# Kernel tuning notes

Hardware: AMD Instinct MI355X
Metric: run time of the kernel (lower is better)

The kernel has to match this reference:

```python
import jax, jax.numpy as jnp
import numpy as np
import math

SEQ = 2048
N_EMBD = 2048
N_HEAD = 16
DIM = N_EMBD // N_HEAD  # 128


def setup_inputs() -> dict:
    key = jax.random.key(0)
    k1, k2, k3, k4, k5 = jax.random.split(key, 5)
    s = 1.0 / math.sqrt(N_EMBD)
    return {
        "hidden_states": jax.random.normal(k1, (SEQ, N_EMBD), dtype=jnp.float32),
        "Wqkv": jax.random.normal(k2, (N_HEAD, N_EMBD, 3 * DIM), dtype=jnp.float32) * s,
        "bqkv": jax.random.normal(k3, (N_HEAD, 3 * DIM), dtype=jnp.float32) * 0.02,
        "Wout": jax.random.normal(k4, (N_EMBD, N_EMBD), dtype=jnp.float32) * s,
        "bout": jax.random.normal(k5, (N_EMBD,), dtype=jnp.float32) * 0.02,
    }


def reference(hidden_states, Wqkv, bqkv, Wout, bout):
    # per-head qkv projection: [h, s, 3*dim]
    qkv = jnp.einsum("se,hed->hsd", hidden_states, Wqkv) + bqkv[:, None, :]
    q, k, v = qkv[..., :DIM], qkv[..., DIM:2 * DIM], qkv[..., 2 * DIM:]
    # NOTE: original divides by sqrt(n_embd), not sqrt(head_dim)
    scale = 1.0 / math.sqrt(N_EMBD)
    scores = jnp.einsum("hsd,htd->hst", q, k) * scale  # [h, s, s]
    causal = jnp.tril(jnp.ones((SEQ, SEQ), dtype=bool))
    scores = jnp.where(causal[None], scores, -jnp.inf)
    probs = jax.nn.softmax(scores, axis=-1)
    out = jnp.einsum("hst,htd->hsd", probs, v)  # [h, s, dim]
    out = jnp.transpose(out, (1, 0, 2)).reshape(SEQ, N_EMBD)  # concat heads
    return out @ Wout + bout
```

## Files before the change

### kernel.cpp

```cpp
#include <hip/hip_runtime.h>
#include <cfloat>

#define SEQ   2048
#define NE    2048
#define NH    16
#define DIM   128
#define NKV   384
#define QSCALE 0.022097086912079611f

typedef __attribute__((ext_vector_type(8))) short bf16x8;
typedef __attribute__((ext_vector_type(4))) float f32x4;
typedef __attribute__((ext_vector_type(16))) float f32x16;
typedef __attribute__((ext_vector_type(8))) unsigned short u16x8;
typedef __attribute__((ext_vector_type(4))) unsigned int u32x4;
typedef __attribute__((ext_vector_type(2))) unsigned int u32x2;

#define PSLOT_B 16896u
#define NUNITS  768

__device__ __forceinline__ unsigned short f32_to_bf16_rn(float x) {
    unsigned u = __builtin_bit_cast(unsigned, x);
    u += 0x7fffu + ((u >> 16) & 1u);
    return (unsigned short)(u >> 16);
}

__device__ __forceinline__ unsigned cvt_pk_bf16(float lo, float hi) {
    unsigned r;
    asm("v_cvt_pk_bf16_f32 %0, %1, %2" : "=v"(r) : "v"(lo), "v"(hi));
    return r;
}
__device__ __forceinline__ float bf16lo(unsigned w) {
    return __builtin_bit_cast(float, w << 16);
}
__device__ __forceinline__ float bf16hi(unsigned w) {
    return __builtin_bit_cast(float, w & 0xFFFF0000u);
}

__device__ __forceinline__ void gload16(const void* g, void* l) {
    __builtin_amdgcn_global_load_lds(
        (const __attribute__((address_space(1))) unsigned int*)g,
        (__attribute__((address_space(3))) unsigned int*)l, 16, 0, 0);
}

__global__ __launch_bounds__(256) void convert_bf16_kernel(
    const float* __restrict__ src, unsigned short* __restrict__ dst, int n4)
{
    for (int i = blockIdx.x * 256 + threadIdx.x; i < n4; i += gridDim.x * 256) {
        float4 x = ((const float4*)src)[i];
        ushort4 h;
        h.x = f32_to_bf16_rn(x.x);
        h.y = f32_to_bf16_rn(x.y);
        h.z = f32_to_bf16_rn(x.z);
        h.w = f32_to_bf16_rn(x.w);
        ((ushort4*)dst)[i] = h;
    }
}

__global__ __launch_bounds__(256) void transpose_bf16_kernel(
    const float* __restrict__ src, unsigned short* __restrict__ dst, int K, int N)
{
    const int kt = blockIdx.x, nt = blockIdx.y, b = blockIdx.z;
    const float* s = src + (size_t)b * K * N;
    __shared__ float tile[64][65];
    const int tid = threadIdx.x;
    #pragma unroll
    for (int i = 0; i < 4; i++) {
        int idx = tid + 256 * i;
        int kk = idx >> 4, n4 = idx & 15;
        float4 val = *(const float4*)&s[(size_t)(kt * 64 + kk) * N + nt * 64 + n4 * 4];
        tile[kk][n4 * 4 + 0] = val.x; tile[kk][n4 * 4 + 1] = val.y;
        tile[kk][n4 * 4 + 2] = val.z; tile[kk][n4 * 4 + 3] = val.w;
    }
    __syncthreads();
    #pragma unroll
    for (int i = 0; i < 2; i++) {
        int idx = tid + 256 * i;
        int nn = idx >> 3, k8 = idx & 7;
        u16x8 hv;
        #pragma unroll
        for (int j = 0; j < 8; j++)
            hv[j] = f32_to_bf16_rn(tile[k8 * 8 + j][nn]);
        size_t off = ((size_t)b * N + nt * 64 + nn) * K + kt * 64 + k8 * 8;
        *(u16x8*)&dst[off] = hv;
    }
}

__global__ __launch_bounds__(256, 4) void gemm_qkv_kernel(
    const unsigned short* __restrict__ A, const unsigned short* __restrict__ B,
    const float* __restrict__ bias,
    unsigned short* __restrict__ o0, unsigned short* __restrict__ o1,
    unsigned short* __restrict__ o2)
{
    __shared__ unsigned short smem[2][128][64];
    const int tid = threadIdx.x;
    const int wave = tid >> 6, lane = tid & 63;
    const int s0 = blockIdx.x * 128, n0 = blockIdx.y * 128, z = blockIdx.z;
    const int bRowBase = z * NKV + n0;

    const int srow = lane >> 3;
    const int sswz = ((lane & 7) ^ srow) << 4;
    size_t aoff[4], boff[4];
    #pragma unroll
    for (int j = 0; j < 4; j++) {
        int ra = s0 + wave * 32 + j * 8 + srow;
        int rb = bRowBase + wave * 32 + j * 8 + srow;
        aoff[j] = 2 * ((size_t)ra * NE) + sswz;
        boff[j] = 2 * ((size_t)rb * NE) + sswz;
    }
    const char* pA = (const char*)A;
    const char* pB = (const char*)B;

    f32x4 acc[4][4];
    #pragma unroll
    for (int i = 0; i < 4; i++)
        #pragma unroll
        for (int j = 0; j < 4; j++) acc[i][j] = (f32x4){0.f, 0.f, 0.f, 0.f};

    const int wm = wave >> 1, wn = wave & 1;
    const int fr = lane & 15, kg = lane >> 4;

    for (int k0 = 0; k0 < NE; k0 += 64) {
        #pragma unroll
        for (int j = 0; j < 4; j++) {
            gload16(pA + aoff[j], &smem[0][wave * 32 + j * 8][0]);
            gload16(pB + boff[j], &smem[1][wave * 32 + j * 8][0]);
            aoff[j] += 128; boff[j] += 128;
        }
        __syncthreads();

        #pragma unroll
        for (int kh = 0; kh < 2; kh++) {
            bf16x8 af[4], bf[4];
            #pragma unroll
            for (int f = 0; f < 4; f++) {
                int ra = wm * 64 + f * 16 + fr;
                int ca = ((kh * 4 + kg) ^ (ra & 7)) << 4;
                af[f] = *(const bf16x8*)((const char*)&smem[0][0][0] + ra * 128 + ca);
                int rb = wn * 64 + f * 16 + fr;
                int cb = ((kh * 4 + kg) ^ (rb & 7)) << 4;
                bf[f] = *(const bf16x8*)((const char*)&smem[1][0][0] + rb * 128 + cb);
            }
            #pragma unroll
            for (int fm = 0; fm < 4; fm++)
                #pragma unroll
                for (int fn = 0; fn < 4; fn++)
                    acc[fm][fn] = __builtin_amdgcn_mfma_f32_16x16x32_bf16(
                        af[fm], bf[fn], acc[fm][fn], 0, 0, 0);
        }
        __syncthreads();
    }

    #pragma unroll
    for (int fm = 0; fm < 4; fm++)
        #pragma unroll
        for (int fn = 0; fn < 4; fn++) {
            int col = wn * 64 + fn * 16 + fr;
            int row = wm * 64 + fm * 16 + kg * 4;
            const int seg = n0 >> 7;
            unsigned short* dst = (seg == 0) ? o0 : ((seg == 1) ? o1 : o2);
            const float mult = (seg == 0) ? QSCALE : 1.f;
            float bv = bias[z * NKV + n0 + col];
            #pragma unroll
            for (int r = 0; r < 4; r++)
                dst[((size_t)(z * SEQ + s0 + row + r)) * DIM + col] =
                    f32_to_bf16_rn((acc[fm][fn][r] + bv) * mult);
        }
}

__global__ __launch_bounds__(128, 3) void gemm_out_kernel(
    const unsigned short* __restrict__ A, const unsigned short* __restrict__ B,
    const float* __restrict__ bias, float* __restrict__ out)
{
    __shared__ unsigned short As[64][64];
    __shared__ unsigned short Bs[128][64];
    const int tid = threadIdx.x;
    const int wave = tid >> 6, lane = tid & 63;
    const int s0 = blockIdx.x * 64, n0 = blockIdx.y * 128;

    const int srow = lane >> 3;
    const int sswz = ((lane & 7) ^ srow) << 4;
    size_t aof[4], boff[4], boff2[4];
    #pragma unroll
    for (int j = 0; j < 4; j++) {
        int ra = s0 + wave * 32 + j * 8 + srow;
        aof[j] = 2 * ((size_t)ra * NE) + sswz;
        int rb = n0 + wave * 64 + j * 8 + srow;
        boff[j] = 2 * ((size_t)rb * NE) + sswz;
        int rb2 = n0 + wave * 64 + 32 + j * 8 + srow;
        boff2[j] = 2 * ((size_t)rb2 * NE) + sswz;
    }
    const char* pA = (const char*)A;
    const char* pB = (const char*)B;

    f32x4 acc[4][4];
    #pragma unroll
    for (int i = 0; i < 4; i++)
        #pragma unroll
        for (int j = 0; j < 4; j++) acc[i][j] = (f32x4){0.f, 0.f, 0.f, 0.f};

    const int fr = lane & 15, kg = lane >> 4;

    for (int k0 = 0; k0 < NE; k0 += 64) {
        #pragma unroll
        for (int j = 0; j < 4; j++) {
            gload16(pA + aof[j], &As[wave * 32 + j * 8][0]);
            gload16(pB + boff[j], &Bs[wave * 64 + j * 8][0]);
            gload16(pB + boff2[j], &Bs[wave * 64 + 32 + j * 8][0]);
            aof[j] += 128; boff[j] += 128; boff2[j] += 128;
        }
        __syncthreads();

        #pragma unroll
        for (int kh = 0; kh < 2; kh++) {
            bf16x8 af[4], bf[4];
            #pragma unroll
            for (int f = 0; f < 4; f++) {
                int ra = f * 16 + fr;
                int ca = ((kh * 4 + kg) ^ (ra & 7)) << 4;
                af[f] = *(const bf16x8*)((const char*)&As[0][0] + ra * 128 + ca);
                int rb = wave * 64 + f * 16 + fr;
                int cb = ((kh * 4 + kg) ^ (rb & 7)) << 4;
                bf[f] = *(const bf16x8*)((const char*)&Bs[0][0] + rb * 128 + cb);
            }
            #pragma unroll
            for (int fm = 0; fm < 4; fm++)
                #pragma unroll
                for (int fn = 0; fn < 4; fn++)
                    acc[fm][fn] = __builtin_amdgcn_mfma_f32_16x16x32_bf16(
                        af[fm], bf[fn], acc[fm][fn], 0, 0, 0);
        }
        __syncthreads();
    }

    #pragma unroll
    for (int fm = 0; fm < 4; fm++)
        #pragma unroll
        for (int fn = 0; fn < 4; fn++) {
            int col = n0 + wave * 64 + fn * 16 + fr;
            int row = s0 + fm * 16 + kg * 4;
            float bv = bias[col];
            #pragma unroll
            for (int r = 0; r < 4; r++)
                out[(size_t)(row + r) * NE + col] = acc[fm][fn][r] + bv;
        }
}

__global__ __launch_bounds__(128, 2) void attn_partial_kernel(
    const unsigned short* __restrict__ Qb, const unsigned short* __restrict__ Kb,
    const unsigned short* __restrict__ Vb, char* __restrict__ partB,
    unsigned short* __restrict__ AOb)
{
    const int uid = (int)blockIdx.x;
    const int h = uid & 15;
    const int u = uid >> 4;
    int qt, t_begin, t_end, chunk;
    bool direct;
    if (u < 16) {
        qt = 16 + u; t_begin = 0; t_end = 16; chunk = 0; direct = false;
    } else {
        int p = (u - 16) >> 1;
        if (((u - 16) & 1) == 0) { qt = 15 - p; t_begin = 0; t_end = qt + 1; chunk = 0; direct = true; }
        else                     { qt = 31 - p; t_begin = 16; t_end = qt + 1; chunk = 1; direct = false; }
    }
    char* slotB = partB + (size_t)((h * 16 + (qt - 16)) * 2 + chunk) * PSLOT_B;

    const char* kh = (const char*)(Kb + (size_t)h * SEQ * DIM);
    const unsigned short* vh = Vb + (size_t)h * SEQ * DIM;

    __shared__ __align__(16) unsigned short Klds[64 * 128];
    __shared__ __align__(16) unsigned short Vt[128][72];

    const int tid = threadIdx.x;
    const int w = tid >> 6, lane = tid & 63;
    const int cc = lane & 31, hh = lane >> 5;
    const int Q0 = qt * 64 + w * 32;

    bf16x8 qf[8];
    {
        const unsigned short* qrow = Qb + ((size_t)h * SEQ + Q0 + cc) * DIM;
        #pragma unroll
        for (int st = 0; st < 8; st++)
            qf[st] = *(const bf16x8*)&qrow[st * 16 + hh * 8];
    }

    const int key0 = (tid & 31) * 2;
    const int dbase = (tid >> 5) * 32;

    f32x16 oacc[4];
    #pragma unroll
    for (int dt = 0; dt < 4; dt++)
        #pragma unroll
        for (int r = 0; r < 16; r++) oacc[dt][r] = 0.f;
    float m_run = -FLT_MAX, l_run = 0.f;

    u16x8 vrA[4], vrB[4];

    {
        const int tb0 = t_begin * 64;
        #pragma unroll
        for (int j = 0; j < 8; j++) {
            int row = w * 32 + j * 4 + (lane >> 4);
            gload16(kh + (size_t)(tb0 + row) * 256 + (((lane & 15) ^ (row & 7)) << 4),
                    &Klds[(w * 32 + j * 4) * 128]);
        }
        const u16x8* p0 = (const u16x8*)&vh[(size_t)(tb0 + key0) * DIM + dbase];
        const u16x8* p1 = (const u16x8*)&vh[(size_t)(tb0 + key0 + 1) * DIM + dbase];
        #pragma unroll
        for (int q8 = 0; q8 < 4; q8++) { vrA[q8] = p0[q8]; vrB[q8] = p1[q8]; }
        #pragma unroll
        for (int q8 = 0; q8 < 4; q8++)
            #pragma unroll
            for (int j = 0; j < 8; j++)
                *(unsigned*)&Vt[dbase + q8 * 8 + j][key0] =
                    (unsigned)(unsigned short)vrA[q8][j] |
                    ((unsigned)(unsigned short)vrB[q8][j] << 16);
        asm volatile("s_waitcnt vmcnt(0)" ::: "memory");
        __syncthreads();
    }

    for (int t = t_begin; t < t_end; t++) {
        const int t0 = t * 64;
        const bool notlast = (t + 1 < t_end);
        const int t1 = t0 + 64;

        if (notlast) {
            const u16x8* p0 = (const u16x8*)&vh[(size_t)(t1 + key0) * DIM + dbase];
            const u16x8* p1 = (const u16x8*)&vh[(size_t)(t1 + key0 + 1) * DIM + dbase];
            #pragma unroll
            for (int q8 = 0; q8 < 4; q8++) { vrA[q8] = p0[q8]; vrB[q8] = p1[q8]; }
        }

        f32x16 s0, s1;
        #pragma unroll
        for (int r = 0; r < 16; r++) { s0[r] = 0.f; s1[r] = 0.f; }
        __builtin_amdgcn_s_setprio(1);
        #pragma unroll
        for (int st = 0; st < 8; st++) {
            int r0 = cc, r1 = 32 + cc;
            bf16x8 kf0 = *(const bf16x8*)((const char*)&Klds[0] +
                            r0 * 256 + (((2 * st + hh) ^ (r0 & 7)) << 4));
            bf16x8 kf1 = *(const bf16x8*)((const char*)&Klds[0] +
                            r1 * 256 + (((2 * st + hh) ^ (r1 & 7)) << 4));
            s0 = __builtin_amdgcn_mfma_f32_32x32x16_bf16(kf0, qf[st], s0, 0, 0, 0);
            s1 = __builtin_amdgcn_mfma_f32_32x32x16_bf16(kf1, qf[st], s1, 0, 0, 0);
        }
        __builtin_amdgcn_s_setprio(0);

        if (t == qt) {
            const int q = Q0 + cc;
            #pragma unroll
            for (int r = 0; r < 16; r++) {
                int krow = (r & 3) + 8 * (r >> 2) + 4 * hh;
                s0[r] = (t0 + krow > q) ? -3.0e38f : s0[r];
                s1[r] = (t0 + 32 + krow > q) ? -3.0e38f : s1[r];
            }
        }

        float t4[4];
        #pragma unroll
        for (int j = 0; j < 4; j++) t4[j] = fmaxf(s0[j], s1[j]);
        #pragma unroll
        for (int r = 4; r < 16; r++) t4[r & 3] = fmaxf(t4[r & 3], fmaxf(s0[r], s1[r]));
        float mx = fmaxf(fmaxf(t4[0], t4[1]), fmaxf(t4[2], t4[3]));
        mx = fmaxf(mx, __shfl_xor(mx, 32));
        const bool nog = __all((int)(mx - m_run <= 8.f));
        float sc = 1.f;
        if (!nog) {
            float m_new = fmaxf(m_run, mx);
            sc = __expf(m_run - m_new);
            m_run = m_new;
        }

        float e4[4] = {0.f, 0.f, 0.f, 0.f};
        #pragma unroll
        for (int r = 0; r < 16; r++) {
            s0[r] = __expf(s0[r] - m_run);
            s1[r] = __expf(s1[r] - m_run);
            e4[r & 3] += s0[r] + s1[r];
        }
        float psum = (e4[0] + e4[1]) + (e4[2] + e4[3]);
        psum += __shfl_xor(psum, 32);
        l_run = l_run * sc + psum;
        if (!nog) {
            #pragma unroll
            for (int dt = 0; dt < 4; dt++)
                #pragma unroll
                for (int r = 0; r < 16; r++) oacc[dt][r] *= sc;
        }

        unsigned pd[16];
        #pragma unroll
        for (int uu = 0; uu < 8; uu++) {
            pd[uu]     = cvt_pk_bf16(s0[2 * uu], s0[2 * uu + 1]);
            pd[8 + uu] = cvt_pk_bf16(s1[2 * uu], s1[2 * uu + 1]);
        }

        __builtin_amdgcn_s_setprio(1);
        #pragma unroll
        for (int km = 0; km < 4; km++) {
            u32x2 sA = __builtin_amdgcn_permlane32_swap(pd[4 * km + 0], pd[4 * km + 2], false, false);
            u32x2 sB = __builtin_amdgcn_permlane32_swap(pd[4 * km + 1], pd[4 * km + 3], false, false);
            u32x4 pw; pw[0] = sA[0]; pw[1] = sB[0]; pw[2] = sA[1]; pw[3] = sB[1];
            bf16x8 pb = __builtin_bit_cast(bf16x8, pw);
            #pragma unroll
            for (int dt = 0; dt < 4; dt++) {
                bf16x8 vf = *(const bf16x8*)&Vt[dt * 32 + cc][km * 16 + hh * 8];
                oacc[dt] = __builtin_amdgcn_mfma_f32_32x32x16_bf16(vf, pb, oacc[dt], 0, 0, 0);
            }
        }
        __builtin_amdgcn_s_setprio(0);

        if (notlast) {
            __syncthreads();
            #pragma unroll
            for (int j = 0; j < 8; j++) {
                int row = w * 32 + j * 4 + (lane >> 4);
                gload16(kh + (size_t)(t1 + row) * 256 + (((lane & 15) ^ (row & 7)) << 4),
                        &Klds[(w * 32 + j * 4) * 128]);
            }
            #pragma unroll
            for (int q8 = 0; q8 < 4; q8++)
                #pragma unroll
                for (int j = 0; j < 8; j++)
                    *(unsigned*)&Vt[dbase + q8 * 8 + j][key0] =
                        (unsigned)(unsigned short)vrA[q8][j] |
                        ((unsigned)(unsigned short)vrB[q8][j] << 16);
            asm volatile("s_waitcnt vmcnt(0)" ::: "memory");
            __syncthreads();
        }
    }

    const int prow = w * 32 + cc;
    const float inv = 1.f / l_run;
    if (direct) {
        unsigned short* aorow = AOb + (size_t)(Q0 + cc) * NE + h * DIM;
        #pragma unroll
        for (int dt = 0; dt < 4; dt++)
            #pragma unroll
            for (int m = 0; m < 4; m++) {
                unsigned lo = cvt_pk_bf16(oacc[dt][4 * m + 0] * inv, oacc[dt][4 * m + 1] * inv);
                unsigned hi = cvt_pk_bf16(oacc[dt][4 * m + 2] * inv, oacc[dt][4 * m + 3] * inv);
                u32x2 pk; pk[0] = lo; pk[1] = hi;
                *(u32x2*)&aorow[dt * 32 + 8 * m + 4 * hh] = pk;
            }
    } else {
        float* mf = (float*)slotB;
        float* lf = mf + 64;
        if (hh == 0) { mf[prow] = m_run; lf[prow] = l_run; }
        unsigned short* orow = (unsigned short*)(slotB + 512) + (size_t)prow * 128;
        #pragma unroll
        for (int dt = 0; dt < 4; dt++)
            #pragma unroll
            for (int m = 0; m < 4; m++) {
                unsigned lo = cvt_pk_bf16(oacc[dt][4 * m + 0] * inv, oacc[dt][4 * m + 1] * inv);
                unsigned hi = cvt_pk_bf16(oacc[dt][4 * m + 2] * inv, oacc[dt][4 * m + 3] * inv);
                u32x2 pk; pk[0] = lo; pk[1] = hi;
                *(u32x2*)&orow[dt * 32 + 8 * m + 4 * hh] = pk;
            }
    }
}

__global__ __launch_bounds__(128) void attn_merge_kernel(
    const char* __restrict__ partB, unsigned short* __restrict__ AOb)
{
    const int blk = (int)blockIdx.x;
    const int h = blk >> 4, qtm = blk & 15;
    const char* s0B = partB + (size_t)((h * 16 + qtm) * 2) * PSLOT_B;
    const char* s1B = s0B + PSLOT_B;
    const float* m0 = (const float*)s0B; const float* l0 = m0 + 64;
    const float* m1 = (const float*)s1B; const float* l1 = m1 + 64;
    const unsigned short* O0 = (const unsigned short*)(s0B + 512);
    const unsigned short* O1 = (const unsigned short*)(s1B + 512);

    const int tid = threadIdx.x;
    const int f4 = tid & 31;
    const int rg = tid >> 5;

    #pragma unroll 1
    for (int j = 0; j < 16; j++) {
        const int row = rg + 4 * j;
        float M = fmaxf(m0[row], m1[row]);
        float w0 = __expf(m0[row] - M) * l0[row];
        float w1 = __expf(m1[row] - M) * l1[row];
        float inv = 1.f / (w0 + w1);
        w0 *= inv; w1 *= inv;
        u32x2 a = *(const u32x2*)&O0[(size_t)row * 128 + f4 * 4];
        u32x2 b = *(const u32x2*)&O1[(size_t)row * 128 + f4 * 4];
        float r0 = w0 * bf16lo(a[0]) + w1 * bf16lo(b[0]);
        float r1 = w0 * bf16hi(a[0]) + w1 * bf16hi(b[0]);
        float r2 = w0 * bf16lo(a[1]) + w1 * bf16lo(b[1]);
        float r3 = w0 * bf16hi(a[1]) + w1 * bf16hi(b[1]);
        u32x2 pk; pk[0] = cvt_pk_bf16(r0, r1); pk[1] = cvt_pk_bf16(r2, r3);
        *(u32x2*)&AOb[(size_t)((16 + qtm) * 64 + row) * NE + h * DIM + f4 * 4] = pk;
    }
}

extern "C" void kernel_launch(void* const* d_in, const int* in_sizes, int n_in,
                              void* d_out, int out_size, void* d_ws, size_t ws_size,
                              hipStream_t stream) {
    const float* H    = (const float*)d_in[0];
    const float* Wqkv = (const float*)d_in[1];
    const float* bqkv = (const float*)d_in[2];
    const float* Wout = (const float*)d_in[3];
    const float* bout = (const float*)d_in[4];
    float* out = (float*)d_out;

    char* W8 = (char*)d_ws;
    const size_t MiB = 1ull << 20;
    unsigned short* qb  = (unsigned short*)(W8 + 0);
    unsigned short* kb  = (unsigned short*)(W8 + 8 * MiB);
    unsigned short* vb  = (unsigned short*)(W8 + 16 * MiB);
    unsigned short* Wob = (unsigned short*)(W8 + 24 * MiB);
    unsigned short* AOb = (unsigned short*)(W8 + 32 * MiB);
    char* part          = (char*)(W8 + 40 * MiB);
    unsigned short* Hb  = (unsigned short*)(W8 + 49 * MiB);
    unsigned short* Wqb = (unsigned short*)(W8 + 57 * MiB);

    convert_bf16_kernel<<<1024, 256, 0, stream>>>(H, Hb, SEQ * NE / 4);
    transpose_bf16_kernel<<<dim3(NE / 64, NKV / 64, NH), 256, 0, stream>>>(
        Wqkv, Wqb, NE, NKV);
    transpose_bf16_kernel<<<dim3(NE / 64, NE / 64, 1), 256, 0, stream>>>(
        Wout, Wob, NE, NE);
    gemm_qkv_kernel<<<dim3(SEQ / 128, NKV / 128, NH), 256, 0, stream>>>(
        Hb, Wqb, bqkv, qb, kb, vb);
    attn_partial_kernel<<<dim3(NUNITS), 128, 0, stream>>>(qb, kb, vb, part, AOb);
    attn_merge_kernel<<<dim3(256), 128, 0, stream>>>(part, AOb);
    gemm_out_kernel<<<dim3(SEQ / 64, NE / 128), 128, 0, stream>>>(
        AOb, Wob, bout, out);
}
```

Baseline: 167.8 us.

## Enlarge attention query tile to 128 rows with 4 waves sharing K/V tiles

The attention partial kernel now processes 128 query rows per block with 256 threads instead of 64 rows with 128 threads. Each K/V tile loaded into LDS is reused by four waves rather than two, which halves global K/V traffic and the number of blocks. The causal mask condition, partial-slot layout and merge kernel are adjusted for the larger tile. In exchange there are fewer blocks (384), coarser load balancing across the causal triangle, and more masked work on diagonal tiles.

Result: slower. 190.9 us (+13.8%).

```diff
diff --git a/kernel.cpp b/kernel.cpp
--- a/kernel.cpp
+++ b/kernel.cpp
@@ -15,8 +15,8 @@
 typedef __attribute__((ext_vector_type(4))) unsigned int u32x4;
 typedef __attribute__((ext_vector_type(2))) unsigned int u32x2;
 
-#define PSLOT_B 16896u
-#define NUNITS  768
+#define PSLOT_B 33792u
+#define NUNITS  384
 
 __device__ __forceinline__ unsigned short f32_to_bf16_rn(float x) {
     unsigned u = __builtin_bit_cast(unsigned, x);
@@ -245,7 +245,7 @@
         }
 }
 
-__global__ __launch_bounds__(128, 2) void attn_partial_kernel(
+__global__ __launch_bounds__(256, 3) void attn_partial_kernel(
     const unsigned short* __restrict__ Qb, const unsigned short* __restrict__ Kb,
     const unsigned short* __restrict__ Vb, char* __restrict__ partB,
     unsigned short* __restrict__ AOb)
@@ -253,16 +253,17 @@
     const int uid = (int)blockIdx.x;
     const int h = uid & 15;
     const int u = uid >> 4;
-    int qt, t_begin, t_end, chunk;
+    int qb, t_begin, t_end, chunk;
     bool direct;
-    if (u < 16) {
-        qt = 16 + u; t_begin = 0; t_end = 16; chunk = 0; direct = false;
+    if (u < 8) {
+        qb = 8 + u; t_begin = 0; t_end = 16; chunk = 0; direct = false;
     } else {
-        int p = (u - 16) >> 1;
-        if (((u - 16) & 1) == 0) { qt = 15 - p; t_begin = 0; t_end = qt + 1; chunk = 0; direct = true; }
-        else                     { qt = 31 - p; t_begin = 16; t_end = qt + 1; chunk = 1; direct = false; }
-    }
-    char* slotB = partB + (size_t)((h * 16 + (qt - 16)) * 2 + chunk) * PSLOT_B;
+        int p = (u - 8) >> 1;
+        if (((u - 8) & 1) == 0) { qb = 7 - p;  t_begin = 0;  t_end = 2 * qb + 2; chunk = 0; direct = true; }
+        else                    { qb = 15 - p; t_begin = 16; t_end = 2 * qb + 2; chunk = 1; direct = false; }
+    }
+    const int sidx = direct ? 0 : ((h * 8 + (qb - 8)) * 2 + chunk);
+    char* slotB = partB + (size_t)sidx * PSLOT_B;
 
     const char* kh = (const char*)(Kb + (size_t)h * SEQ * DIM);
     const unsigned short* vh = Vb + (size_t)h * SEQ * DIM;
@@ -273,7 +274,7 @@
     const int tid = threadIdx.x;
     const int w = tid >> 6, lane = tid & 63;
     const int cc = lane & 31, hh = lane >> 5;
-    const int Q0 = qt * 64 + w * 32;
+    const int Q0 = qb * 128 + w * 32;
 
     bf16x8 qf[8];
     {
@@ -284,7 +285,7 @@
     }
 
     const int key0 = (tid & 31) * 2;
-    const int dbase = (tid >> 5) * 32;
+    const int dbase = (tid >> 5) * 16;
 
     f32x16 oacc[4];
     #pragma unroll
@@ -293,27 +294,26 @@
         for (int r = 0; r < 16; r++) oacc[dt][r] = 0.f;
     float m_run = -FLT_MAX, l_run = 0.f;
 
-    u16x8 vrA[4], vrB[4];
+    u16x8 vrA[2], vrB[2];
 
     {
         const int tb0 = t_begin * 64;
         #pragma unroll
-        for (int j = 0; j < 8; j++) {
-            int row = w * 32 + j * 4 + (lane >> 4);
+        for (int j = 0; j < 4; j++) {
+            int row = w * 16 + j * 4 + (lane >> 4);
             gload16(kh + (size_t)(tb0 + row) * 256 + (((lane & 15) ^ (row & 7)) << 4),
-                    &Klds[(w * 32 + j * 4) * 128]);
+                    &Klds[(w * 16 + j * 4) * 128]);
         }
         const u16x8* p0 = (const u16x8*)&vh[(size_t)(tb0 + key0) * DIM + dbase];
         const u16x8* p1 = (const u16x8*)&vh[(size_t)(tb0 + key0 + 1) * DIM + dbase];
-        #pragma unroll
-        for (int q8 = 0; q8 < 4; q8++) { vrA[q8] = p0[q8]; vrB[q8] = p1[q8]; }
-        #pragma unroll
-        for (int q8 = 0; q8 < 4; q8++)
+        vrA[0] = p0[0]; vrA[1] = p0[1]; vrB[0] = p1[0]; vrB[1] = p1[1];
+        #pragma unroll
+        for (int g = 0; g < 2; g++)
             #pragma unroll
             for (int j = 0; j < 8; j++)
-                *(unsigned*)&Vt[dbase + q8 * 8 + j][key0] =
-                    (unsigned)(unsigned short)vrA[q8][j] |
-                    ((unsigned)(unsigned short)vrB[q8][j] << 16);
+                *(unsigned*)&Vt[dbase + g * 8 + j][key0] =
+                    (unsigned)(unsigned short)vrA[g][j] |
+                    ((unsigned)(unsigned short)vrB[g][j] << 16);
         asm volatile("s_waitcnt vmcnt(0)" ::: "memory");
         __syncthreads();
     }
@@ -326,8 +326,7 @@
         if (notlast) {
             const u16x8* p0 = (const u16x8*)&vh[(size_t)(t1 + key0) * DIM + dbase];
             const u16x8* p1 = (const u16x8*)&vh[(size_t)(t1 + key0 + 1) * DIM + dbase];
-            #pragma unroll
-            for (int q8 = 0; q8 < 4; q8++) { vrA[q8] = p0[q8]; vrB[q8] = p1[q8]; }
+            vrA[0] = p0[0]; vrA[1] = p0[1]; vrB[0] = p1[0]; vrB[1] = p1[1];
         }
 
         f32x16 s0, s1;
@@ -346,7 +345,7 @@
         }
         __builtin_amdgcn_s_setprio(0);
 
-        if (t == qt) {
+        if (t0 + 63 > Q0) {
             const int q = Q0 + cc;
             #pragma unroll
             for (int r = 0; r < 16; r++) {
@@ -413,18 +412,18 @@
         if (notlast) {
             __syncthreads();
             #pragma unroll
-            for (int j = 0; j < 8; j++) {
-                int row = w * 32 + j * 4 + (lane >> 4);
+            for (int j = 0; j < 4; j++) {
+                int row = w * 16 + j * 4 + (lane >> 4);
                 gload16(kh + (size_t)(t1 + row) * 256 + (((lane & 15) ^ (row & 7)) << 4),
-                        &Klds[(w * 32 + j * 4) * 128]);
-            }
-            #pragma unroll
-            for (int q8 = 0; q8 < 4; q8++)
+                        &Klds[(w * 16 + j * 4) * 128]);
+            }
+            #pragma unroll
+            for (int g = 0; g < 2; g++)
                 #pragma unroll
                 for (int j = 0; j < 8; j++)
-                    *(unsigned*)&Vt[dbase + q8 * 8 + j][key0] =
-                        (unsigned)(unsigned short)vrA[q8][j] |
-                        ((unsigned)(unsigned short)vrB[q8][j] << 16);
+                    *(unsigned*)&Vt[dbase + g * 8 + j][key0] =
+                        (unsigned)(unsigned short)vrA[g][j] |
+                        ((unsigned)(unsigned short)vrB[g][j] << 16);
             asm volatile("s_waitcnt vmcnt(0)" ::: "memory");
             __syncthreads();
         }
@@ -445,9 +444,9 @@
             }
     } else {
         float* mf = (float*)slotB;
-        float* lf = mf + 64;
+        float* lf = mf + 128;
         if (hh == 0) { mf[prow] = m_run; lf[prow] = l_run; }
-        unsigned short* orow = (unsigned short*)(slotB + 512) + (size_t)prow * 128;
+        unsigned short* orow = (unsigned short*)(slotB + 1024) + (size_t)prow * 128;
         #pragma unroll
         for (int dt = 0; dt < 4; dt++)
             #pragma unroll
@@ -464,20 +463,20 @@
     const char* __restrict__ partB, unsigned short* __restrict__ AOb)
 {
     const int blk = (int)blockIdx.x;
-    const int h = blk >> 4, qtm = blk & 15;
-    const char* s0B = partB + (size_t)((h * 16 + qtm) * 2) * PSLOT_B;
+    const int h = blk >> 3, qbm = blk & 7;
+    const char* s0B = partB + (size_t)((h * 8 + qbm) * 2) * PSLOT_B;
     const char* s1B = s0B + PSLOT_B;
-    const float* m0 = (const float*)s0B; const float* l0 = m0 + 64;
-    const float* m1 = (const float*)s1B; const float* l1 = m1 + 64;
-    const unsigned short* O0 = (const unsigned short*)(s0B + 512);
-    const unsigned short* O1 = (const unsigned short*)(s1B + 512);
+    const float* m0 = (const float*)s0B; const float* l0 = m0 + 128;
+    const float* m1 = (const float*)s1B; const float* l1 = m1 + 128;
+    const unsigned short* O0 = (const unsigned short*)(s0B + 1024);
+    const unsigned short* O1 = (const unsigned short*)(s1B + 1024);
 
     const int tid = threadIdx.x;
     const int f4 = tid & 31;
     const int rg = tid >> 5;
 
     #pragma unroll 1
-    for (int j = 0; j < 16; j++) {
+    for (int j = 0; j < 32; j++) {
         const int row = rg + 4 * j;
         float M = fmaxf(m0[row], m1[row]);
         float w0 = __expf(m0[row] - M) * l0[row];
@@ -491,7 +490,7 @@
         float r2 = w0 * bf16lo(a[1]) + w1 * bf16lo(b[1]);
         float r3 = w0 * bf16hi(a[1]) + w1 * bf16hi(b[1]);
         u32x2 pk; pk[0] = cvt_pk_bf16(r0, r1); pk[1] = cvt_pk_bf16(r2, r3);
-        *(u32x2*)&AOb[(size_t)((16 + qtm) * 64 + row) * NE + h * DIM + f4 * 4] = pk;
+        *(u32x2*)&AOb[(size_t)((8 + qbm) * 128 + row) * NE + h * DIM + f4 * 4] = pk;
     }
 }
 
@@ -523,8 +522,8 @@
         Wout, Wob, NE, NE);
     gemm_qkv_kernel<<<dim3(SEQ / 128, NKV / 128, NH), 256, 0, stream>>>(
         Hb, Wqb, bqkv, qb, kb, vb);
-    attn_partial_kernel<<<dim3(NUNITS), 128, 0, stream>>>(qb, kb, vb, part, AOb);
-    attn_merge_kernel<<<dim3(256), 128, 0, stream>>>(part, AOb);
+    attn_partial_kernel<<<dim3(NUNITS), 256, 0, stream>>>(qb, kb, vb, part, AOb);
+    attn_merge_kernel<<<dim3(128), 128, 0, stream>>>(part, AOb);
     gemm_out_kernel<<<dim3(SEQ / 64, NE / 128), 128, 0, stream>>>(
         AOb, Wob, bout, out);
 }
```

## Emit V pre-transposed from QKV GEMM and async-load it; fuse prep kernels

Applied to the files above, without the earlier changes.

The QKV GEMM epilogue now writes V in a head-major transposed [dim][seq] layout. The attention kernel can then stream V tiles straight into swizzled LDS with global_load_lds, instead of loading into registers and transposing through scalar LDS stores each iteration. The three input conversion and transpose kernels are also merged into one launch to cut launch overhead. The trade-offs are V epilogue stores that are strided along SEQ, and a larger bf16-to-fp32 conversion blob in a single kernel.

Measured after the change: 159.3 us. 5.1% less time.

```diff
diff --git a/kernel.cpp b/kernel.cpp
--- a/kernel.cpp
+++ b/kernel.cpp
@@ -42,32 +42,15 @@
         (__attribute__((address_space(3))) unsigned int*)l, 16, 0, 0);
 }
 
-__global__ __launch_bounds__(256) void convert_bf16_kernel(
-    const float* __restrict__ src, unsigned short* __restrict__ dst, int n4)
+__device__ __forceinline__ void transpose_tile_64(
+    const float* __restrict__ src, unsigned short* __restrict__ dst,
+    int K, int N, int kt, int nt, float (*tile)[65], int tid)
 {
-    for (int i = blockIdx.x * 256 + threadIdx.x; i < n4; i += gridDim.x * 256) {
-        float4 x = ((const float4*)src)[i];
-        ushort4 h;
-        h.x = f32_to_bf16_rn(x.x);
-        h.y = f32_to_bf16_rn(x.y);
-        h.z = f32_to_bf16_rn(x.z);
-        h.w = f32_to_bf16_rn(x.w);
-        ((ushort4*)dst)[i] = h;
-    }
-}
-
-__global__ __launch_bounds__(256) void transpose_bf16_kernel(
-    const float* __restrict__ src, unsigned short* __restrict__ dst, int K, int N)
-{
-    const int kt = blockIdx.x, nt = blockIdx.y, b = blockIdx.z;
-    const float* s = src + (size_t)b * K * N;
-    __shared__ float tile[64][65];
-    const int tid = threadIdx.x;
     #pragma unroll
     for (int i = 0; i < 4; i++) {
         int idx = tid + 256 * i;
         int kk = idx >> 4, n4 = idx & 15;
-        float4 val = *(const float4*)&s[(size_t)(kt * 64 + kk) * N + nt * 64 + n4 * 4];
+        float4 val = *(const float4*)&src[(size_t)(kt * 64 + kk) * N + nt * 64 + n4 * 4];
         tile[kk][n4 * 4 + 0] = val.x; tile[kk][n4 * 4 + 1] = val.y;
         tile[kk][n4 * 4 + 2] = val.z; tile[kk][n4 * 4 + 3] = val.w;
     }
@@ -80,8 +63,44 @@
         #pragma unroll
         for (int j = 0; j < 8; j++)
             hv[j] = f32_to_bf16_rn(tile[k8 * 8 + j][nn]);
-        size_t off = ((size_t)b * N + nt * 64 + nn) * K + kt * 64 + k8 * 8;
+        size_t off = (size_t)(nt * 64 + nn) * K + kt * 64 + k8 * 8;
         *(u16x8*)&dst[off] = hv;
+    }
+}
+
+__global__ __launch_bounds__(256) void prep_kernel(
+    const float* __restrict__ H, const float* __restrict__ Wqkv,
+    const float* __restrict__ Wout,
+    unsigned short* __restrict__ Hb, unsigned short* __restrict__ Wqb,
+    unsigned short* __restrict__ Wob)
+{
+    __shared__ float tile[64][65];
+    const int b = (int)blockIdx.x;
+    const int tid = threadIdx.x;
+    if (b < 1024) {
+        const int n4 = SEQ * NE / 4;
+        for (int i = b * 256 + tid; i < n4; i += 1024 * 256) {
+            float4 x = ((const float4*)H)[i];
+            ushort4 h;
+            h.x = f32_to_bf16_rn(x.x);
+            h.y = f32_to_bf16_rn(x.y);
+            h.z = f32_to_bf16_rn(x.z);
+            h.w = f32_to_bf16_rn(x.w);
+            ((ushort4*)Hb)[i] = h;
+        }
+    } else if (b < 4096) {
+        const int idx = b - 1024;
+        const int kt = idx & 31;
+        const int nt = (idx >> 5) % 6;
+        const int hh = (idx >> 5) / 6;
+        transpose_tile_64(Wqkv + (size_t)hh * NE * NKV,
+                          Wqb + (size_t)hh * NKV * NE,
+                          NE, NKV, kt, nt, tile, tid);
+    } else {
+        const int idx = b - 4096;
+        const int kt = idx & 31;
+        const int nt = idx >> 5;
+        transpose_tile_64(Wout, Wob, NE, NE, kt, nt, tile, tid);
     }
 }
 
@@ -150,20 +169,27 @@
         __syncthreads();
     }
 
+    const int seg = n0 >> 7;
     #pragma unroll
     for (int fm = 0; fm < 4; fm++)
         #pragma unroll
         for (int fn = 0; fn < 4; fn++) {
             int col = wn * 64 + fn * 16 + fr;
             int row = wm * 64 + fm * 16 + kg * 4;
-            const int seg = n0 >> 7;
-            unsigned short* dst = (seg == 0) ? o0 : ((seg == 1) ? o1 : o2);
-            const float mult = (seg == 0) ? QSCALE : 1.f;
             float bv = bias[z * NKV + n0 + col];
-            #pragma unroll
-            for (int r = 0; r < 4; r++)
-                dst[((size_t)(z * SEQ + s0 + row + r)) * DIM + col] =
-                    f32_to_bf16_rn((acc[fm][fn][r] + bv) * mult);
+            if (seg == 2) {
+                unsigned lo = cvt_pk_bf16(acc[fm][fn][0] + bv, acc[fm][fn][1] + bv);
+                unsigned hi = cvt_pk_bf16(acc[fm][fn][2] + bv, acc[fm][fn][3] + bv);
+                u32x2 pk; pk[0] = lo; pk[1] = hi;
+                *(u32x2*)&o2[((size_t)z * DIM + col) * SEQ + s0 + row] = pk;
+            } else {
+                unsigned short* dst = (seg == 0) ? o0 : o1;
+                const float mult = (seg == 0) ? QSCALE : 1.f;
+                #pragma unroll
+                for (int r = 0; r < 4; r++)
+                    dst[((size_t)(z * SEQ + s0 + row + r)) * DIM + col] =
+                        f32_to_bf16_rn((acc[fm][fn][r] + bv) * mult);
+            }
         }
 }
 
@@ -247,7 +273,7 @@
 
 __global__ __launch_bounds__(128, 2) void attn_partial_kernel(
     const unsigned short* __restrict__ Qb, const unsigned short* __restrict__ Kb,
-    const unsigned short* __restrict__ Vb, char* __restrict__ partB,
+    const unsigned short* __restrict__ VTb, char* __restrict__ partB,
     unsigned short* __restrict__ AOb)
 {
     const int uid = (int)blockIdx.x;
@@ -264,11 +290,11 @@
     }
     char* slotB = partB + (size_t)((h * 16 + (qt - 16)) * 2 + chunk) * PSLOT_B;
 
-    const char* kh = (const char*)(Kb + (size_t)h * SEQ * DIM);
-    const unsigned short* vh = Vb + (size_t)h * SEQ * DIM;
+    const char* kh  = (const char*)(Kb + (size_t)h * SEQ * DIM);
+    const char* vth = (const char*)(VTb + (size_t)h * DIM * SEQ);
 
     __shared__ __align__(16) unsigned short Klds[64 * 128];
-    __shared__ __align__(16) unsigned short Vt[128][72];
+    __shared__ __align__(16) unsigned short Vt[128 * 64];
 
     const int tid = threadIdx.x;
     const int w = tid >> 6, lane = tid & 63;
@@ -283,8 +309,10 @@
             qf[st] = *(const bf16x8*)&qrow[st * 16 + hh * 8];
     }
 
-    const int key0 = (tid & 31) * 2;
-    const int dbase = (tid >> 5) * 32;
+    const int k_row4 = lane >> 4;
+    const int k_slot = lane & 15;
+    const int v_row8 = lane >> 3;
+    const int v_slot = lane & 7;
 
     f32x16 oacc[4];
     #pragma unroll
@@ -293,27 +321,20 @@
         for (int r = 0; r < 16; r++) oacc[dt][r] = 0.f;
     float m_run = -FLT_MAX, l_run = 0.f;
 
-    u16x8 vrA[4], vrB[4];
-
     {
         const int tb0 = t_begin * 64;
         #pragma unroll
         for (int j = 0; j < 8; j++) {
-            int row = w * 32 + j * 4 + (lane >> 4);
-            gload16(kh + (size_t)(tb0 + row) * 256 + (((lane & 15) ^ (row & 7)) << 4),
+            int row = w * 32 + j * 4 + k_row4;
+            gload16(kh + (size_t)(tb0 + row) * 256 + ((k_slot ^ (row & 7)) << 4),
                     &Klds[(w * 32 + j * 4) * 128]);
         }
-        const u16x8* p0 = (const u16x8*)&vh[(size_t)(tb0 + key0) * DIM + dbase];
-        const u16x8* p1 = (const u16x8*)&vh[(size_t)(tb0 + key0 + 1) * DIM + dbase];
-        #pragma unroll
-        for (int q8 = 0; q8 < 4; q8++) { vrA[q8] = p0[q8]; vrB[q8] = p1[q8]; }
-        #pragma unroll
-        for (int q8 = 0; q8 < 4; q8++)
-            #pragma unroll
-            for (int j = 0; j < 8; j++)
-                *(unsigned*)&Vt[dbase + q8 * 8 + j][key0] =
-                    (unsigned)(unsigned short)vrA[q8][j] |
-                    ((unsigned)(unsigned short)vrB[q8][j] << 16);
+        #pragma unroll
+        for (int j = 0; j < 8; j++) {
+            int row = w * 64 + j * 8 + v_row8;
+            gload16(vth + (size_t)row * (SEQ * 2) + tb0 * 2 + ((v_slot ^ (row & 7)) << 4),
+                    &Vt[(w * 64 + j * 8) * 64]);
+        }
         asm volatile("s_waitcnt vmcnt(0)" ::: "memory");
         __syncthreads();
     }
@@ -322,13 +343,6 @@
         const int t0 = t * 64;
         const bool notlast = (t + 1 < t_end);
         const int t1 = t0 + 64;
-
-        if (notlast) {
-            const u16x8* p0 = (const u16x8*)&vh[(size_t)(t1 + key0) * DIM + dbase];
-            const u16x8* p1 = (const u16x8*)&vh[(size_t)(t1 + key0 + 1) * DIM + dbase];
-            #pragma unroll
-            for (int q8 = 0; q8 < 4; q8++) { vrA[q8] = p0[q8]; vrB[q8] = p1[q8]; }
-        }
 
         f32x16 s0, s1;
         #pragma unroll
@@ -404,7 +418,9 @@
             bf16x8 pb = __builtin_bit_cast(bf16x8, pw);
             #pragma unroll
             for (int dt = 0; dt < 4; dt++) {
-                bf16x8 vf = *(const bf16x8*)&Vt[dt * 32 + cc][km * 16 + hh * 8];
+                int d = dt * 32 + cc;
+                bf16x8 vf = *(const bf16x8*)((const char*)&Vt[0] +
+                                d * 128 + (((km * 2 + hh) ^ (d & 7)) << 4));
                 oacc[dt] = __builtin_amdgcn_mfma_f32_32x32x16_bf16(vf, pb, oacc[dt], 0, 0, 0);
             }
         }
@@ -414,17 +430,16 @@
             __syncthreads();
             #pragma unroll
             for (int j = 0; j < 8; j++) {
-                int row = w * 32 + j * 4 + (lane >> 4);
-                gload16(kh + (size_t)(t1 + row) * 256 + (((lane & 15) ^ (row & 7)) << 4),
+                int row = w * 32 + j * 4 + k_row4;
+                gload16(kh + (size_t)(t1 + row) * 256 + ((k_slot ^ (row & 7)) << 4),
                         &Klds[(w * 32 + j * 4) * 128]);
             }
             #pragma unroll
-            for (int q8 = 0; q8 < 4; q8++)
-                #pragma unroll
-                for (int j = 0; j < 8; j++)
-                    *(unsigned*)&Vt[dbase + q8 * 8 + j][key0] =
-                        (unsigned)(unsigned short)vrA[q8][j] |
-                        ((unsigned)(unsigned short)vrB[q8][j] << 16);
+            for (int j = 0; j < 8; j++) {
+                int row = w * 64 + j * 8 + v_row8;
+                gload16(vth + (size_t)row * (SEQ * 2) + t1 * 2 + ((v_slot ^ (row & 7)) << 4),
+                        &Vt[(w * 64 + j * 8) * 64]);
+            }
             asm volatile("s_waitcnt vmcnt(0)" ::: "memory");
             __syncthreads();
         }
@@ -509,21 +524,17 @@
     const size_t MiB = 1ull << 20;
     unsigned short* qb  = (unsigned short*)(W8 + 0);
     unsigned short* kb  = (unsigned short*)(W8 + 8 * MiB);
-    unsigned short* vb  = (unsigned short*)(W8 + 16 * MiB);
+    unsigned short* vtb = (unsigned short*)(W8 + 16 * MiB);
     unsigned short* Wob = (unsigned short*)(W8 + 24 * MiB);
     unsigned short* AOb = (unsigned short*)(W8 + 32 * MiB);
     char* part          = (char*)(W8 + 40 * MiB);
     unsigned short* Hb  = (unsigned short*)(W8 + 49 * MiB);
     unsigned short* Wqb = (unsigned short*)(W8 + 57 * MiB);
 
-    convert_bf16_kernel<<<1024, 256, 0, stream>>>(H, Hb, SEQ * NE / 4);
-    transpose_bf16_kernel<<<dim3(NE / 64, NKV / 64, NH), 256, 0, stream>>>(
-        Wqkv, Wqb, NE, NKV);
-    transpose_bf16_kernel<<<dim3(NE / 64, NE / 64, 1), 256, 0, stream>>>(
-        Wout, Wob, NE, NE);
+    prep_kernel<<<dim3(5120), 256, 0, stream>>>(H, Wqkv, Wout, Hb, Wqb, Wob);
     gemm_qkv_kernel<<<dim3(SEQ / 128, NKV / 128, NH), 256, 0, stream>>>(
-        Hb, Wqb, bqkv, qb, kb, vb);
-    attn_partial_kernel<<<dim3(NUNITS), 128, 0, stream>>>(qb, kb, vb, part, AOb);
+        Hb, Wqb, bqkv, qb, kb, vtb);
+    attn_partial_kernel<<<dim3(NUNITS), 128, 0, stream>>>(qb, kb, vtb, part, AOb);
     attn_merge_kernel<<<dim3(256), 128, 0, stream>>>(part, AOb);
     gemm_out_kernel<<<dim3(SEQ / 64, NE / 128), 128, 0, stream>>>(
         AOb, Wob, bout, out);
```
